# Kernel tuning notes

Hardware: AMD Instinct MI355X
Metric: run time of the kernel (lower is better)

## Reference

```python
import jax, jax.numpy as jnp
import numpy as np

D_MODEL = 1024
N_HEADS = 16
D_K = D_MODEL // N_HEADS
BATCH = 4
SEQ = 2048


def setup_inputs() -> dict:
    key = jax.random.key(0)
    ks = jax.random.split(key, 12)
    s = 1.0 / np.sqrt(D_MODEL)
    inp = {
        "context_sequence": jax.random.normal(ks[0], (BATCH, SEQ, D_MODEL), jnp.float32),
        "value_sequence": jax.random.normal(ks[1], (BATCH, SEQ, D_MODEL), jnp.float32),
        # True = masked (causal: cannot attend to future positions)
        "mask": jnp.triu(jnp.ones((SEQ, SEQ), dtype=bool), k=1),
        "Wq": jax.random.uniform(ks[2], (D_MODEL, D_MODEL), jnp.float32, -s, s),
        "bq": jax.random.uniform(ks[3], (D_MODEL,), jnp.float32, -s, s),
        "Wk": jax.random.uniform(ks[4], (D_MODEL, D_MODEL), jnp.float32, -s, s),
        "bk": jax.random.uniform(ks[5], (D_MODEL,), jnp.float32, -s, s),
        "Wv": jax.random.uniform(ks[6], (D_MODEL, D_MODEL), jnp.float32, -s, s),
        "bv": jax.random.uniform(ks[7], (D_MODEL,), jnp.float32, -s, s),
        "Wo": jax.random.uniform(ks[8], (D_MODEL, D_MODEL), jnp.float32, -s, s),
        "bo": jax.random.uniform(ks[9], (D_MODEL,), jnp.float32, -s, s),
    }
    return inp


def reference(context_sequence, value_sequence, mask, Wq, bq, Wk, bk, Wv, bv, Wo, bo):
    B, S, _ = context_sequence.shape
    # projections; split heads: [B, H, S, Dk]
    def split_heads(x):
        return x.reshape(B, S, N_HEADS, D_K).transpose(0, 2, 1, 3)

    Q = split_heads(context_sequence @ Wq + bq)
    K = split_heads(context_sequence @ Wk + bk)
    V = split_heads(value_sequence @ Wv + bv)

    scale = 1.0 / jnp.sqrt(jnp.asarray(D_K, dtype=Q.dtype))
    scores = jnp.einsum("bhqd,bhkd->bhqk", Q, K) * scale  # [B,H,S,S]
    scores = jnp.where(mask, jnp.asarray(-1e9, dtype=scores.dtype), scores)
    attn = jax.nn.softmax(scores, axis=-1)
    out = jnp.einsum("bhqk,bhkd->bhqd", attn, V)
    out = out.transpose(0, 2, 1, 3).reshape(B, S, D_MODEL)
    return out @ Wo + bo  # dropout p=0 (eval) -> identity
```

## Files before the change

### kernel.cpp

```cpp
#include <hip/hip_runtime.h>
#include <stdint.h>

#define D_MODEL 1024
#define SEQ 2048
#define BATCH 4
#define NH 16
#define DK 64

typedef float f32x4 __attribute__((ext_vector_type(4)));
typedef float f32x16 __attribute__((ext_vector_type(16)));
typedef __bf16 bf16x8 __attribute__((ext_vector_type(8)));
typedef unsigned short us4v __attribute__((ext_vector_type(4)));

__device__ __forceinline__ unsigned short f2bf(float f) {
  union { float f; unsigned u; } x; x.f = f;
  unsigned r = x.u + 0x7FFFu + ((x.u >> 16) & 1u);
  return (unsigned short)(r >> 16);
}

__device__ __forceinline__ void gll16(const void* g, void* l) {
  __builtin_amdgcn_global_load_lds(
      (__attribute__((address_space(1))) void*)g,
      (__attribute__((address_space(3))) void*)l, 16, 0, 0);
}

__device__ __forceinline__ int cvtpk(float lo, float hi) {
  int r;
  asm("v_cvt_pk_bf16_f32 %0, %1, %2" : "=v"(r) : "v"(lo), "v"(hi));
  return r;
}
__device__ __forceinline__ void pl32swap(int& a, int& b) {
  asm volatile("v_permlane32_swap_b32 %0, %1" : "+v"(a), "+v"(b));
}
__device__ __forceinline__ float xmax32(float x) {
  int a = __float_as_int(x), b;
  asm volatile("v_mov_b32 %0, %1" : "=v"(b) : "v"(a));
  pl32swap(a, b);
  return fmaxf(__int_as_float(a), __int_as_float(b));
}
__device__ __forceinline__ float exp2fast(float x) {
  float r;
  asm("v_exp_f32 %0, %1" : "=v"(r) : "v"(x));
  return r;
}

__global__ void cvtbf2(const float* __restrict__ a, const float* __restrict__ b,
                       unsigned short* __restrict__ out, const int nseg) {
  const int t = blockIdx.x * blockDim.x + threadIdx.x;
  const int stride = gridDim.x * blockDim.x;
  for (int i = t * 4; i < 2 * nseg; i += stride * 4) {
    const float* src = (i < nseg) ? &a[i] : &b[i - nseg];
    const float4 v = *(const float4*)src;
    us4v o;
    o[0] = f2bf(v.x); o[1] = f2bf(v.y); o[2] = f2bf(v.z); o[3] = f2bf(v.w);
    *(us4v*)&out[i] = o;
  }
}

__global__ void wtrans(const float* __restrict__ W0, const float* __restrict__ W1,
                       const float* __restrict__ W2, const float* __restrict__ W3,
                       unsigned short* __restrict__ T0, unsigned short* __restrict__ T1,
                       unsigned short* __restrict__ T2, unsigned short* __restrict__ T3) {
  __shared__ float t[32][33];
  const int z = blockIdx.z;
  const float* W = (z == 0) ? W0 : (z == 1) ? W1 : (z == 2) ? W2 : W3;
  unsigned short* T = (z == 0) ? T0 : (z == 1) ? T1 : (z == 2) ? T2 : T3;
  const int n0 = blockIdx.x * 32, k0 = blockIdx.y * 32;
  const int tx = threadIdx.x, ty = threadIdx.y;
#pragma unroll
  for (int i = 0; i < 4; ++i)
    t[ty + 8 * i][tx] = W[(size_t)(k0 + ty + 8 * i) * D_MODEL + n0 + tx];
  __syncthreads();
#pragma unroll
  for (int i = 0; i < 4; ++i)
    T[(size_t)(n0 + ty + 8 * i) * D_MODEL + k0 + tx] = f2bf(t[tx][ty + 8 * i]);
}

__device__ __forceinline__ void gemm_body(
    const unsigned short* __restrict__ A, const unsigned short* __restrict__ Bt,
    const float* __restrict__ bias, unsigned short* __restrict__ outb,
    float* __restrict__ outf, const int mode,
    unsigned short* Alds, unsigned short* Blds) {
  const int tid = threadIdx.x;
  const int lane = tid & 63;
  const int w = tid >> 6;
  const int wr = w >> 1, wc = w & 1;

  int flat = (int)blockIdx.x + 8 * (int)blockIdx.y;
  flat = (flat & 7) * 64 + (flat >> 3);
  const int n0 = (flat & 7) * 128;
  const int m0 = (flat >> 3) * 128;

  const int srow = tid >> 3, sslot = tid & 7;

  auto stage = [&](int kk, int buf) {
#pragma unroll
    for (int i = 0; i < 4; ++i) {
      const int r = srow + 32 * i;
      const int gc = kk * 64 + ((sslot ^ (r & 7)) << 3);
      gll16(A + (size_t)(m0 + r) * D_MODEL + gc, &Alds[buf * 8192 + tid * 8 + i * 2048]);
      gll16(Bt + (size_t)(n0 + r) * D_MODEL + gc, &Blds[buf * 8192 + tid * 8 + i * 2048]);
    }
  };

  f32x4 acc[4][4] = {};

  stage(0, 0);
  stage(1, 1);

  const int NK = D_MODEL / 64;
  for (int kk = 0; kk < NK; ++kk) {
    const int cur = kk & 1;
    if (kk + 1 < NK) asm volatile("s_waitcnt vmcnt(8)" ::: "memory");
    else             asm volatile("s_waitcnt vmcnt(0)" ::: "memory");
    __builtin_amdgcn_s_barrier();
    asm volatile("" ::: "memory");

    const unsigned short* Al = &Alds[cur * 8192];
    const unsigned short* Bl = &Blds[cur * 8192];
#pragma unroll
    for (int kf = 0; kf < 2; ++kf) {
      const int sb = kf * 4 + (lane >> 4);
      bf16x8 a[4], b[4];
#pragma unroll
      for (int m = 0; m < 4; ++m) {
        const int row = wr * 64 + m * 16 + (lane & 15);
        a[m] = *(const bf16x8*)&Al[row * 64 + ((sb ^ (row & 7)) << 3)];
      }
#pragma unroll
      for (int n = 0; n < 4; ++n) {
        const int row = wc * 64 + n * 16 + (lane & 15);
        b[n] = *(const bf16x8*)&Bl[row * 64 + ((sb ^ (row & 7)) << 3)];
      }
#pragma unroll
      for (int m = 0; m < 4; ++m)
#pragma unroll
        for (int n = 0; n < 4; ++n)
          acc[m][n] = __builtin_amdgcn_mfma_f32_16x16x32_bf16(a[m], b[n], acc[m][n], 0, 0, 0);
    }

    asm volatile("" ::: "memory");
    __builtin_amdgcn_s_barrier();

    if (kk + 2 < NK) stage(kk + 2, cur);
  }

#pragma unroll
  for (int m = 0; m < 4; ++m) {
    const int rb = m0 + wr * 64 + m * 16 + ((lane >> 4) << 2);
#pragma unroll
    for (int n = 0; n < 4; ++n) {
      const int col = n0 + wc * 64 + n * 16 + (lane & 15);
      const float bv = bias[col];
#pragma unroll
      for (int j = 0; j < 4; ++j) {
        const int row = rb + j;
        const float v = acc[m][n][j] + bv;
        if (mode == 2) {
          outf[(size_t)row * D_MODEL + col] = v;
        } else {
          const int b_ = row >> 11, s_ = row & (SEQ - 1);
          const int h_ = col >> 6, d_ = col & (DK - 1);
          size_t idx;
          if (mode == 0) idx = (((size_t)(b_ * NH + h_)) * SEQ + s_) * DK + d_;
          else           idx = (((size_t)(b_ * NH + h_)) * DK + d_) * SEQ + s_;
          outb[idx] = f2bf(v);
        }
      }
    }
  }
}

__global__ __launch_bounds__(256) void gemmQKV(
    const unsigned short* __restrict__ Xc, const unsigned short* __restrict__ Xv,
    const unsigned short* __restrict__ Wqt, const unsigned short* __restrict__ Wkt,
    const unsigned short* __restrict__ Wvt,
    const float* __restrict__ bq, const float* __restrict__ bk,
    const float* __restrict__ bv,
    unsigned short* __restrict__ Qb, unsigned short* __restrict__ Kb,
    unsigned short* __restrict__ Vtb) {
  __shared__ __align__(16) unsigned short Alds[2 * 128 * 64];
  __shared__ __align__(16) unsigned short Blds[2 * 128 * 64];
  const int z = blockIdx.z;
  const unsigned short* A = (z == 2) ? Xv : Xc;
  const unsigned short* Bt = (z == 0) ? Wqt : (z == 1) ? Wkt : Wvt;
  const float* bias = (z == 0) ? bq : (z == 1) ? bk : bv;
  unsigned short* outb = (z == 0) ? Qb : (z == 1) ? Kb : Vtb;
  gemm_body(A, Bt, bias, outb, nullptr, (z == 2) ? 1 : 0, Alds, Blds);
}

__global__ __launch_bounds__(256) void gemmO(
    const unsigned short* __restrict__ A, const unsigned short* __restrict__ Bt,
    const float* __restrict__ bias, float* __restrict__ outf) {
  __shared__ __align__(16) unsigned short Alds[2 * 128 * 64];
  __shared__ __align__(16) unsigned short Blds[2 * 128 * 64];
  gemm_body(A, Bt, bias, nullptr, outf, 2, Alds, Blds);
}

__global__ __launch_bounds__(256, 3) void attn4w(
    const unsigned short* __restrict__ Q, const unsigned short* __restrict__ K,
    const unsigned short* __restrict__ Vt, unsigned short* __restrict__ O) {
  __shared__ __align__(16) unsigned short Klds[3 * 64 * 64];
  __shared__ __align__(16) unsigned short Vlds[3 * 64 * 64];

  const int tid = threadIdx.x, lane = tid & 63, w = tid >> 6;
  const int lq = lane & 31, hi = lane >> 5;
  const int bh = blockIdx.x;
  const int strip = 15 - (int)blockIdx.y;
  const size_t qkbase = (size_t)bh * SEQ * DK;
  const size_t vbase = (size_t)bh * DK * SEQ;
  const int srow = tid >> 3, sslot = tid & 7;
  const int b_ = bh >> 4, h_ = bh & (NH - 1);

  const int q0 = strip * 128;
  const int qw0 = q0 + w * 32;
  const int qg = qw0 + lq;
  const int n = 2 * strip + 2;

  auto stageKV = [&](int t, int slot) {
#pragma unroll
    for (int i = 0; i < 2; ++i) {
      const int r = srow + 32 * i;
      const int sc = (sslot ^ (r & 7)) << 3;
      gll16(K + qkbase + (size_t)(t * 64 + r) * DK + sc,
            &Klds[slot * 4096 + tid * 8 + i * 2048]);
      gll16(Vt + vbase + (size_t)r * SEQ + t * 64 + sc,
            &Vlds[slot * 4096 + tid * 8 + i * 2048]);
    }
  };

  bf16x8 qb[4];
  {
    const float QSCALE = 0.125f * 1.44269504f;
    const unsigned short* qp = Q + qkbase + (size_t)qg * DK + hi * 8;
#pragma unroll
    for (int ks = 0; ks < 4; ++ks) {
      qb[ks] = *(const bf16x8*)(qp + ks * 16);
#pragma unroll
      for (int e = 0; e < 8; ++e)
        qb[ks][e] = (__bf16)((float)qb[ks][e] * QSCALE);
    }
  }

  float m = -3e38f, l = 0.f;
  f32x16 o0 = {}, o1 = {};

  stageKV(0, 0);
  stageKV(1, 1);

  for (int jt = 0; jt < n; ++jt) {
    const int slot = jt % 3;
    if (jt + 1 < n) asm volatile("s_waitcnt vmcnt(4)" ::: "memory");
    else            asm volatile("s_waitcnt vmcnt(0)" ::: "memory");
    __builtin_amdgcn_s_barrier();
    asm volatile("" ::: "memory");

    if (jt + 2 < n) stageKV(jt + 2, (jt + 2) % 3);

    if (64 * jt < qw0 + 32) {
      const unsigned short* Kl = &Klds[slot * 4096];
      const unsigned short* Vl = &Vlds[slot * 4096];

      f32x16 st0 = {}, st1 = {};
      __builtin_amdgcn_s_setprio(1);
#pragma unroll
      for (int ks = 0; ks < 4; ++ks) {
        const int so = ((ks * 2 + hi) ^ (lq & 7)) << 3;
        const bf16x8 ka0 = *(const bf16x8*)&Kl[lq * 64 + so];
        const bf16x8 ka1 = *(const bf16x8*)&Kl[(32 + lq) * 64 + so];
        st0 = __builtin_amdgcn_mfma_f32_32x32x16_bf16(ka0, qb[ks], st0, 0, 0, 0);
        st1 = __builtin_amdgcn_mfma_f32_32x32x16_bf16(ka1, qb[ks], st1, 0, 0, 0);
      }
      __builtin_amdgcn_s_setprio(0);

      if (64 * jt + 63 > qw0) {
        const int rb = 64 * jt + 4 * hi - qg;
#pragma unroll
        for (int r = 0; r < 16; ++r) {
          const int crow0 = (r & 3) + 8 * (r >> 2);
          if (crow0 + rb > 0)      st0[r] = -3e38f;
          if (crow0 + 32 + rb > 0) st1[r] = -3e38f;
        }
      }

      float tmax[8];
#pragma unroll
      for (int r = 0; r < 8; ++r)
        tmax[r] = fmaxf(fmaxf(st0[r], st0[r + 8]), fmaxf(st1[r], st1[r + 8]));
      float mx = fmaxf(fmaxf(fmaxf(tmax[0], tmax[1]), fmaxf(tmax[2], tmax[3])),
                       fmaxf(fmaxf(tmax[4], tmax[5]), fmaxf(tmax[6], tmax[7])));
      mx = xmax32(mx);

      if (__any((int)(mx > m + 11.5416f))) {
        const float mnew = fmaxf(m, mx);
        const float alpha = exp2fast(m - mnew);
        m = mnew;
        l *= alpha;
#pragma unroll
        for (int r = 0; r < 16; ++r) { o0[r] *= alpha; o1[r] *= alpha; }
      }

#pragma unroll
      for (int r = 0; r < 16; ++r) {
        st0[r] = exp2fast(st0[r] - m);
        st1[r] = exp2fast(st1[r] - m);
      }

      float tsum[8];
#pragma unroll
      for (int r = 0; r < 8; ++r)
        tsum[r] = (st0[r] + st0[r + 8]) + (st1[r] + st1[r + 8]);
      l += ((tsum[0] + tsum[1]) + (tsum[2] + tsum[3])) +
           ((tsum[4] + tsum[5]) + (tsum[6] + tsum[7]));

      bf16x8 pb[4];
#pragma unroll
      for (int ks = 0; ks < 4; ++ks) {
        const int base = (ks & 1) * 8;
        float p0, p1, p2, p3, p4, p5, p6, p7;
        if (ks < 2) {
          p0 = st0[base + 0]; p1 = st0[base + 1]; p2 = st0[base + 2]; p3 = st0[base + 3];
          p4 = st0[base + 4]; p5 = st0[base + 5]; p6 = st0[base + 6]; p7 = st0[base + 7];
        } else {
          p0 = st1[base + 0]; p1 = st1[base + 1]; p2 = st1[base + 2]; p3 = st1[base + 3];
          p4 = st1[base + 4]; p5 = st1[base + 5]; p6 = st1[base + 6]; p7 = st1[base + 7];
        }
        int a0 = cvtpk(p0, p1), a1 = cvtpk(p2, p3);
        int a2 = cvtpk(p4, p5), a3 = cvtpk(p6, p7);
        pl32swap(a0, a2);
        pl32swap(a1, a3);
        union { int i[4]; bf16x8 v; } u;
        u.i[0] = a0; u.i[1] = a1; u.i[2] = a2; u.i[3] = a3;
        pb[ks] = u.v;
      }

      __builtin_amdgcn_s_setprio(1);
#pragma unroll
      for (int ks = 0; ks < 4; ++ks) {
        const int so = ((ks * 2 + hi) ^ (lq & 7)) << 3;
        const bf16x8 va0 = *(const bf16x8*)&Vl[lq * 64 + so];
        const bf16x8 va1 = *(const bf16x8*)&Vl[(32 + lq) * 64 + so];
        o0 = __builtin_amdgcn_mfma_f32_32x32x16_bf16(va0, pb[ks], o0, 0, 0, 0);
        o1 = __builtin_amdgcn_mfma_f32_32x32x16_bf16(va1, pb[ks], o1, 0, 0, 0);
      }
      __builtin_amdgcn_s_setprio(0);
    }
    asm volatile("" ::: "memory");
  }

  l += __shfl_xor(l, 32);
  const float rl = 1.0f / l;
  unsigned short* orow = O + (size_t)(b_ * SEQ + qg) * D_MODEL + h_ * DK;
#pragma unroll
  for (int g = 0; g < 4; ++g) {
    us4v pk0, pk1;
#pragma unroll
    for (int j = 0; j < 4; ++j) {
      pk0[j] = f2bf(o0[4 * g + j] * rl);
      pk1[j] = f2bf(o1[4 * g + j] * rl);
    }
    const int d0 = 8 * g + 4 * hi;
    *(us4v*)&orow[d0] = pk0;
    *(us4v*)&orow[32 + d0] = pk1;
  }
}

extern "C" void kernel_launch(void* const* d_in, const int* in_sizes, int n_in,
                              void* d_out, int out_size, void* d_ws, size_t ws_size,
                              hipStream_t stream) {
  const float* ctx = (const float*)d_in[0];
  const float* val = (const float*)d_in[1];
  const float* Wq = (const float*)d_in[3];
  const float* bq = (const float*)d_in[4];
  const float* Wk = (const float*)d_in[5];
  const float* bk = (const float*)d_in[6];
  const float* Wv = (const float*)d_in[7];
  const float* bv = (const float*)d_in[8];
  const float* Wo = (const float*)d_in[9];
  const float* bo = (const float*)d_in[10];

  unsigned short* ws = (unsigned short*)d_ws;
  const size_t XSZ = (size_t)BATCH * SEQ * D_MODEL;
  const size_t WSZ = (size_t)D_MODEL * D_MODEL;
  unsigned short* Xc  = ws;
  unsigned short* Xv  = Xc + XSZ;
  unsigned short* Wqt = Xv + XSZ;
  unsigned short* Wkt = Wqt + WSZ;
  unsigned short* Wvt = Wkt + WSZ;
  unsigned short* Wot = Wvt + WSZ;
  unsigned short* Qb  = Wot + WSZ;
  unsigned short* Kb  = Qb + XSZ;
  unsigned short* Vtb = Kb + XSZ;
  unsigned short* Ob  = Vtb + XSZ;

  cvtbf2<<<2048, 256, 0, stream>>>(ctx, val, Xc, (int)XSZ);
  wtrans<<<dim3(32, 32, 4), dim3(32, 8), 0, stream>>>(Wq, Wk, Wv, Wo, Wqt, Wkt, Wvt, Wot);

  gemmQKV<<<dim3(8, 64, 3), 256, 0, stream>>>(Xc, Xv, Wqt, Wkt, Wvt,
                                              bq, bk, bv, Qb, Kb, Vtb);

  attn4w<<<dim3(BATCH * NH, 16), 256, 0, stream>>>(Qb, Kb, Vtb, Ob);

  gemmO<<<dim3(8, 64), 256, 0, stream>>>(Ob, Wot, bo, (float*)d_out);
}
```

Baseline: 169.9 us.

## Merge prep kernels into one launch and split QKV GEMM into three launches

Folds the fp32-to-bf16 activation conversion and the weight transpose into a single prep kernel that picks its role from the block index, saving one launch. The fused QKV GEMM, which used blockIdx.z, becomes three separate launches of a shared gemm128 kernel, which adds launches and removes the chance for Q, K and V tiles to run concurrently. The per-z pointer selects go away in exchange.

```diff
diff --git a/kernel.cpp b/kernel.cpp
--- a/kernel.cpp
+++ b/kernel.cpp
@@ -44,43 +44,50 @@
   return r;
 }
 
-__global__ void cvtbf2(const float* __restrict__ a, const float* __restrict__ b,
-                       unsigned short* __restrict__ out, const int nseg) {
-  const int t = blockIdx.x * blockDim.x + threadIdx.x;
-  const int stride = gridDim.x * blockDim.x;
-  for (int i = t * 4; i < 2 * nseg; i += stride * 4) {
-    const float* src = (i < nseg) ? &a[i] : &b[i - nseg];
-    const float4 v = *(const float4*)src;
-    us4v o;
-    o[0] = f2bf(v.x); o[1] = f2bf(v.y); o[2] = f2bf(v.z); o[3] = f2bf(v.w);
-    *(us4v*)&out[i] = o;
-  }
-}
-
-__global__ void wtrans(const float* __restrict__ W0, const float* __restrict__ W1,
-                       const float* __restrict__ W2, const float* __restrict__ W3,
-                       unsigned short* __restrict__ T0, unsigned short* __restrict__ T1,
-                       unsigned short* __restrict__ T2, unsigned short* __restrict__ T3) {
-  __shared__ float t[32][33];
-  const int z = blockIdx.z;
-  const float* W = (z == 0) ? W0 : (z == 1) ? W1 : (z == 2) ? W2 : W3;
-  unsigned short* T = (z == 0) ? T0 : (z == 1) ? T1 : (z == 2) ? T2 : T3;
-  const int n0 = blockIdx.x * 32, k0 = blockIdx.y * 32;
-  const int tx = threadIdx.x, ty = threadIdx.y;
-#pragma unroll
-  for (int i = 0; i < 4; ++i)
-    t[ty + 8 * i][tx] = W[(size_t)(k0 + ty + 8 * i) * D_MODEL + n0 + tx];
-  __syncthreads();
-#pragma unroll
-  for (int i = 0; i < 4; ++i)
-    T[(size_t)(n0 + ty + 8 * i) * D_MODEL + k0 + tx] = f2bf(t[tx][ty + 8 * i]);
-}
-
-__device__ __forceinline__ void gemm_body(
+__global__ __launch_bounds__(256) void prep(
+    const float* __restrict__ ctx, const float* __restrict__ val,
+    unsigned short* __restrict__ X,
+    const float* __restrict__ W0, const float* __restrict__ W1,
+    const float* __restrict__ W2, const float* __restrict__ W3,
+    unsigned short* __restrict__ T0, unsigned short* __restrict__ T1,
+    unsigned short* __restrict__ T2, unsigned short* __restrict__ T3,
+    const int nseg) {
+  const int blk = blockIdx.x;
+  if (blk < 2048) {
+    const int t = blk * 256 + threadIdx.x;
+    const int stride = 2048 * 256 * 4;
+    for (int i = t * 4; i < 2 * nseg; i += stride) {
+      const float* src = (i < nseg) ? &ctx[i] : &val[i - nseg];
+      const float4 v = *(const float4*)src;
+      us4v o;
+      o[0] = f2bf(v.x); o[1] = f2bf(v.y); o[2] = f2bf(v.z); o[3] = f2bf(v.w);
+      *(us4v*)&X[i] = o;
+    }
+  } else {
+    __shared__ float t[32][33];
+    const int wblk = blk - 2048;
+    const int z = wblk >> 10;
+    const int rem = wblk & 1023;
+    const int n0 = (rem & 31) * 32, k0 = (rem >> 5) * 32;
+    const int tx = threadIdx.x & 31, ty = threadIdx.x >> 5;
+    const float* W = (z == 0) ? W0 : (z == 1) ? W1 : (z == 2) ? W2 : W3;
+    unsigned short* T = (z == 0) ? T0 : (z == 1) ? T1 : (z == 2) ? T2 : T3;
+#pragma unroll
+    for (int i = 0; i < 4; ++i)
+      t[ty + 8 * i][tx] = W[(size_t)(k0 + ty + 8 * i) * D_MODEL + n0 + tx];
+    __syncthreads();
+#pragma unroll
+    for (int i = 0; i < 4; ++i)
+      T[(size_t)(n0 + ty + 8 * i) * D_MODEL + k0 + tx] = f2bf(t[tx][ty + 8 * i]);
+  }
+}
+
+__global__ __launch_bounds__(256) void gemm128(
     const unsigned short* __restrict__ A, const unsigned short* __restrict__ Bt,
     const float* __restrict__ bias, unsigned short* __restrict__ outb,
-    float* __restrict__ outf, const int mode,
-    unsigned short* Alds, unsigned short* Blds) {
+    float* __restrict__ outf, const int mode) {
+  __shared__ __align__(16) unsigned short Alds[2 * 128 * 64];
+  __shared__ __align__(16) unsigned short Blds[2 * 128 * 64];
   const int tid = threadIdx.x;
   const int lane = tid & 63;
   const int w = tid >> 6;
@@ -169,32 +176,6 @@
       }
     }
   }
-}
-
-__global__ __launch_bounds__(256) void gemmQKV(
-    const unsigned short* __restrict__ Xc, const unsigned short* __restrict__ Xv,
-    const unsigned short* __restrict__ Wqt, const unsigned short* __restrict__ Wkt,
-    const unsigned short* __restrict__ Wvt,
-    const float* __restrict__ bq, const float* __restrict__ bk,
-    const float* __restrict__ bv,
-    unsigned short* __restrict__ Qb, unsigned short* __restrict__ Kb,
-    unsigned short* __restrict__ Vtb) {
-  __shared__ __align__(16) unsigned short Alds[2 * 128 * 64];
-  __shared__ __align__(16) unsigned short Blds[2 * 128 * 64];
-  const int z = blockIdx.z;
-  const unsigned short* A = (z == 2) ? Xv : Xc;
-  const unsigned short* Bt = (z == 0) ? Wqt : (z == 1) ? Wkt : Wvt;
-  const float* bias = (z == 0) ? bq : (z == 1) ? bk : bv;
-  unsigned short* outb = (z == 0) ? Qb : (z == 1) ? Kb : Vtb;
-  gemm_body(A, Bt, bias, outb, nullptr, (z == 2) ? 1 : 0, Alds, Blds);
-}
-
-__global__ __launch_bounds__(256) void gemmO(
-    const unsigned short* __restrict__ A, const unsigned short* __restrict__ Bt,
-    const float* __restrict__ bias, float* __restrict__ outf) {
-  __shared__ __align__(16) unsigned short Alds[2 * 128 * 64];
-  __shared__ __align__(16) unsigned short Blds[2 * 128 * 64];
-  gemm_body(A, Bt, bias, nullptr, outf, 2, Alds, Blds);
 }
 
 __global__ __launch_bounds__(256, 3) void attn4w(
@@ -393,13 +374,15 @@
   unsigned short* Vtb = Kb + XSZ;
   unsigned short* Ob  = Vtb + XSZ;
 
-  cvtbf2<<<2048, 256, 0, stream>>>(ctx, val, Xc, (int)XSZ);
-  wtrans<<<dim3(32, 32, 4), dim3(32, 8), 0, stream>>>(Wq, Wk, Wv, Wo, Wqt, Wkt, Wvt, Wot);
-
-  gemmQKV<<<dim3(8, 64, 3), 256, 0, stream>>>(Xc, Xv, Wqt, Wkt, Wvt,
-                                              bq, bk, bv, Qb, Kb, Vtb);
+  prep<<<6144, 256, 0, stream>>>(ctx, val, Xc, Wq, Wk, Wv, Wo,
+                                 Wqt, Wkt, Wvt, Wot, (int)XSZ);
+
+  dim3 gg(D_MODEL / 128, BATCH * SEQ / 128);
+  gemm128<<<gg, 256, 0, stream>>>(Xc, Wqt, bq, Qb, nullptr, 0);
+  gemm128<<<gg, 256, 0, stream>>>(Xc, Wkt, bk, Kb, nullptr, 0);
+  gemm128<<<gg, 256, 0, stream>>>(Xv, Wvt, bv, Vtb, nullptr, 1);
 
   attn4w<<<dim3(BATCH * NH, 16), 256, 0, stream>>>(Qb, Kb, Vtb, Ob);
 
-  gemmO<<<dim3(8, 64), 256, 0, stream>>>(Ob, Wot, bo, (float*)d_out);
-}
+  gemm128<<<gg, 256, 0, stream>>>(Ob, Wot, bo, nullptr, (float*)d_out, 2);
+}
```

New measurement: 176.2 us. +3.7%, slower.
